# Kernel tuning notes

Hardware: AMD Instinct MI355X
Metric: run time of the kernel (lower is better)

Reference implementation:

```python
import jax, jax.numpy as jnp
import numpy as np

N_LAYERS = 2
NUM_BRANCHES = 3
TOPK_START = 10
TOPK_END = 3


def normalize_adj(adj):
    # symmetric degree normalization: D^-1/2 (A + I) D^-1/2
    n = adj.shape[0]
    a = jnp.clip(adj + jnp.eye(n, dtype=adj.dtype), 1e-8, jnp.inf)
    row_sum = jnp.clip(a.sum(axis=1), 1e-8, jnp.inf)
    d = jnp.clip(row_sum ** -0.5, 0.0, 100.0)
    return d[:, None] * a * d[None, :]


def setup_inputs() -> dict:
    key = jax.random.key(0)
    k1, k2 = jax.random.split(key)
    B, T, N, C = 512, 16, 22, 64
    x = jax.random.normal(k1, (B, T, N, C), dtype=jnp.float32)
    # emulate nn.Parameter init: clamp(adj,0,1)*0.01 + 0.05*I
    raw = jax.random.uniform(k2, (N, N), dtype=jnp.float32)
    adj = jnp.clip(raw, 0.0, 1.0) * 0.01 + 0.05 * jnp.eye(N, dtype=jnp.float32)
    branch_temps = jnp.ones((NUM_BRANCHES,), dtype=jnp.float32)
    fusion_logits = jnp.zeros((N_LAYERS, NUM_BRANCHES), dtype=jnp.float32)
    return {"x": x, "adj": adj, "branch_temps": branch_temps, "fusion_logits": fusion_logits}


def reference(x, adj, branch_temps, fusion_logits):
    B, T, N, C = x.shape
    # [B, T, N, C] -> [B, N, T*C]
    x0 = jnp.transpose(x, (0, 2, 1, 3)).reshape(B, N, T * C)
    A = normalize_adj(jnp.clip(adj, 0.0, 1.0))          # [N, N]
    temps = jnp.clip(branch_temps, 0.1, 10.0)           # [nb]
    eye = jnp.eye(N, dtype=x0.dtype)

    xb = x0
    for layer in range(N_LAYERS):
        K = int(TOPK_START - (TOPK_START - TOPK_END) * (layer / max(1, N_LAYERS - 1)))
        K = min(K, N)
        alpha = jax.nn.softmax(fusion_logits[layer])    # [nb]
        # cosine similarity, masked by normalized adjacency
        xn = xb / (jnp.linalg.norm(xb, axis=-1, keepdims=True) + 1e-6)
        sim = jnp.einsum('bnd,bmd->bnm', xn, xn) * A    # [B, N, N]
        # per-branch temperature + diagonal boost
        att = sim[None] / temps[:, None, None, None] + 0.1 * eye  # [nb, B, N, N]
        # annealed top-k sparsification (zeros still participate in softmax, as in torch)
        _, idx = jax.lax.top_k(att, K)                  # [nb, B, N, K]
        mask = jax.nn.one_hot(idx, N, dtype=att.dtype).sum(axis=-2)  # [nb, B, N, N]
        att = jax.nn.softmax(att * mask, axis=-1)
        y = jnp.einsum('kbnm,bmd->kbnd', att, xb)       # branch aggregation
        xb = jnp.einsum('k,kbnd->bnd', alpha, y)        # fusion
        if layer > 0:
            xb = xb + x0
        if layer < N_LAYERS - 1:
            xb = jax.nn.relu(xb)  # dropout identity in eval mode
    return xb, A
```

## Files before the change

kernel.cpp:

```cpp
#include <hip/hip_runtime.h>
#include <hip/hip_bf16.h>

#define BATCH  512
#define TT     16
#define NN     22
#define CC     64
#define DD     1024
#define NB     3
#define NTHR   512
#define WPAD   40

typedef __bf16 bf16x8 __attribute__((ext_vector_type(8)));
typedef float  f32x4  __attribute__((ext_vector_type(4)));
typedef float  f32x16 __attribute__((ext_vector_type(16)));

__device__ __forceinline__ unsigned bf16rne(float x) {
  unsigned u = __float_as_uint(x);
  u += 0x7fffu + ((u >> 16) & 1u);
  return u >> 16;
}
__device__ __forceinline__ unsigned pack2(float a, float b) {
  return bf16rne(a) | (bf16rne(b) << 16);
}
__device__ __forceinline__ unsigned xoff(unsigned m, unsigned d) {
  return ((d >> 4) * 6u + (m >> 2)) * 64u + (m & 3u) * 16u + (d & 15u);
}

__global__ __launch_bounds__(NTHR) void mbdsca_fused(
    const float* __restrict__ x,
    const float* __restrict__ adj,
    const float* __restrict__ btemps,
    const float* __restrict__ flogits,
    float* __restrict__ out)
{
  __shared__ unsigned short xs[6 * 64 * 64];
  __shared__ float As[NN][NN];
  __shared__ float Gp[4][NN][NN];
  __shared__ float simS[NN][NN];
  __shared__ float attB[NB][NN][NN];
  __shared__ float mxs[NB][NN];
  __shared__ float sinv[NB][NN];
  __shared__ unsigned short Wh[32][WPAD];
  __shared__ unsigned short Wl[32][WPAD];
  __shared__ float deg[NN];
  __shared__ float alphas[2][NB];
  __shared__ float tvals[NB];

  const int tid  = threadIdx.x;
  const int b    = blockIdx.x;
  const int lane = tid & 63;
  const int wv   = tid >> 6;

  if (tid < NN * NN) {
    int n = tid / NN, m = tid - n * NN;
    float v = adj[tid];
    v = fminf(fmaxf(v, 0.0f), 1.0f);
    if (n == m) v += 1.0f;
    As[n][m] = fmaxf(v, 1e-8f);
  }
  if (tid < NB) tvals[tid] = fminf(fmaxf(btemps[tid], 0.1f), 10.0f);
  for (int i = tid; i < 32 * WPAD / 2; i += NTHR) {
    ((unsigned*)Wh)[i] = 0u;
    ((unsigned*)Wl)[i] = 0u;
  }
  __syncthreads();

  if (tid < NN) {
    float s = 0.0f;
    for (int m = 0; m < NN; ++m) s += As[tid][m];
    s = fmaxf(s, 1e-8f);
    deg[tid] = fminf(fmaxf(1.0f / sqrtf(s), 0.0f), 100.0f);
  }
  if (tid == 0) {
    for (int l = 0; l < 2; ++l) {
      float l0 = flogits[l*NB+0], l1 = flogits[l*NB+1], l2 = flogits[l*NB+2];
      float mx = fmaxf(l0, fmaxf(l1, l2));
      float e0 = __expf(l0-mx), e1 = __expf(l1-mx), e2 = __expf(l2-mx);
      float s = e0 + e1 + e2;
      alphas[l][0] = e0/s; alphas[l][1] = e1/s; alphas[l][2] = e2/s;
    }
  }
  __syncthreads();

  if (tid < NN * NN) {
    int n = tid / NN, m = tid - n * NN;
    As[n][m] = deg[n] * As[n][m] * deg[m];
  }
  #pragma unroll
  for (int j = 0; j < 11; ++j) {
    int f4  = tid + j * NTHR;
    int t   = f4 / (NN * (CC/4));
    int rem = f4 - t * (NN * (CC/4));
    int n   = rem >> 4;
    int c4  = rem & 15;
    const float4 v = *(const float4*)(&x[(size_t)b * (TT*NN*CC) + (size_t)f4 * 4]);
    uint2 p; p.x = pack2(v.x, v.y); p.y = pack2(v.z, v.w);
    *(uint2*)(&xs[xoff(n, t * 64 + c4 * 4)]) = p;
  }
  {
    int m  = 22 + (tid >> 8);
    int d0 = (tid & 255) * 4;
    *(uint2*)(&xs[xoff(m, d0)]) = make_uint2(0u, 0u);
  }
  __syncthreads();

  const unsigned xsb = (unsigned)(unsigned long long)(void*)&xs[0];

  for (int layer = 0; layer < 2; ++layer) {
    const int K = (layer == 0) ? 10 : 3;

    if (wv < 4) {
      int row = lane & 31; if (row > NN-1) row = NN-1;
      const int hi = lane >> 5;
      f32x16 acc0 = {}, acc1 = {};
      #pragma unroll
      for (int s = 0; s < 16; ++s) {
        int d0 = (wv * 16 + s) * 16 + hi * 8;
        bf16x8 a = *(const bf16x8*)(&xs[xoff(row, d0)]);
        if (s & 1) acc1 = __builtin_amdgcn_mfma_f32_32x32x16_bf16(a, a, acc1, 0, 0, 0);
        else       acc0 = __builtin_amdgcn_mfma_f32_32x32x16_bf16(a, a, acc0, 0, 0, 0);
      }
      #pragma unroll
      for (int r = 0; r < 16; ++r) {
        float vv = acc0[r] + acc1[r];
        int orow = (r & 3) + 8 * (r >> 2) + 4 * hi;
        int ocol = lane & 31;
        if (orow < NN && ocol < NN) Gp[wv][orow][ocol] = vv;
      }
    }
    __syncthreads();

    if (tid < NN * NN) {
      int n = tid / NN, m = tid - n * NN;
      float g  = Gp[0][n][m] + Gp[1][n][m] + Gp[2][n][m] + Gp[3][n][m];
      float gn = Gp[0][n][n] + Gp[1][n][n] + Gp[2][n][n] + Gp[3][n][n];
      float gm = Gp[0][m][m] + Gp[1][m][m] + Gp[2][m][m] + Gp[3][m][m];
      float rn = 1.0f / (sqrtf(gn) + 1e-6f);
      float rm = 1.0f / (sqrtf(gm) + 1e-6f);
      simS[n][m] = g * rn * rm * As[n][m];
    }
    __syncthreads();

    if (tid < NN * NN) {
      const int n = tid / NN, m = tid - n * NN;
      float simrow[NN];
      float simn = 0.f, simm = 0.f, rmax_ex = -1e30f;
      #pragma unroll
      for (int j = 0; j < NN; ++j) {
        float s = simS[n][j];
        simrow[j] = s;
        simn = (j == n) ? s : simn;
        simm = (j == m) ? s : simm;
        rmax_ex = (j == n) ? rmax_ex : fmaxf(rmax_ex, s);
      }
      #pragma unroll
      for (int k = 0; k < NB; ++k) {
        const float tk  = tvals[k];
        const float rtk = 1.0f / tk;
        const float vn  = simn + 0.1f * tk;
        const float vown = (m == n) ? vn : simm;
        int rank = 0;
        #pragma unroll
        for (int j = 0; j < NN; ++j) {
          float vj = (j == n) ? vn : simrow[j];
          rank += (vj > vown) || (vj == vown && j < m);
        }
        attB[k][n][m] = (rank < K) ? vown * rtk : 0.0f;
        if (m == 0) mxs[k][n] = fmaxf(fmaxf(rmax_ex, vn) * rtk, 0.0f);
      }
    }
    __syncthreads();

    if (tid < NB * NN) {
      int k = tid / NN, n = tid - k * NN;
      float mx = mxs[k][n], s = 0.0f;
      #pragma unroll
      for (int m2 = 0; m2 < NN; ++m2) s += __expf(attB[k][n][m2] - mx);
      sinv[k][n] = alphas[layer][k] / s;
    }
    __syncthreads();

    if (tid < NN * NN) {
      int n = tid / NN, m = tid - n * NN;
      float w = 0.0f;
      #pragma unroll
      for (int k = 0; k < NB; ++k)
        w += __expf(attB[k][n][m] - mxs[k][n]) * sinv[k][n];
      unsigned h = bf16rne(w);
      Wh[n][m] = (unsigned short)h;
      Wl[n][m] = (unsigned short)bf16rne(w - __uint_as_float(h << 16));
    }
    __syncthreads();

    {
      const int n_b = lane & 31;
      const int ko  = (lane >> 5) * 8;
      bf16x8 w0h = *(const bf16x8*)(&Wh[n_b][ko]);
      bf16x8 w0l = *(const bf16x8*)(&Wl[n_b][ko]);
      bf16x8 w1h = *(const bf16x8*)(&Wh[n_b][16 + ko]);
      bf16x8 w1l = *(const bf16x8*)(&Wl[n_b][16 + ko]);
      const int dpr     = lane & 31;
      const int dsub_in = dpr >> 4;
      const int dcol    = dpr & 15;
      const int hi5     = lane >> 5;
      unsigned mqA  = (unsigned)(hi5 * 2);
      unsigned mqB0 = 4 + mqA;  if (mqB0 > 5) mqB0 = 5;
      unsigned mqB1 = 5 + mqA;  if (mqB1 > 5) mqB1 = 5;
      #pragma unroll
      for (int i = 0; i < 4; ++i) {
        const int dtile = wv * 4 + i;
        const unsigned rowb = xsb + (unsigned)(dtile * 2 + dsub_in) * 6u * 128u + (unsigned)dcol * 8u;
        unsigned long long t00, t01, t10, t11;
        asm volatile("ds_read_b64_tr_b16 %0, %1" : "=v"(t00) : "v"(rowb + mqA * 128u));
        asm volatile("ds_read_b64_tr_b16 %0, %1" : "=v"(t01) : "v"(rowb + (mqA + 1u) * 128u));
        asm volatile("ds_read_b64_tr_b16 %0, %1" : "=v"(t10) : "v"(rowb + mqB0 * 128u));
        asm volatile("ds_read_b64_tr_b16 %0, %1" : "=v"(t11) : "v"(rowb + mqB1 * 128u));
        asm volatile("s_waitcnt lgkmcnt(0)" ::: "memory");
        __builtin_amdgcn_sched_barrier(0);
        int4 a0i = make_int4((int)t00, (int)(t00 >> 32), (int)t01, (int)(t01 >> 32));
        int4 a1i = make_int4((int)t10, (int)(t10 >> 32), (int)t11, (int)(t11 >> 32));
        bf16x8 A0 = __builtin_bit_cast(bf16x8, a0i);
        bf16x8 A1 = __builtin_bit_cast(bf16x8, a1i);
        f32x16 acc = {};
        acc = __builtin_amdgcn_mfma_f32_32x32x16_bf16(A0, w0h, acc, 0, 0, 0);
        acc = __builtin_amdgcn_mfma_f32_32x32x16_bf16(A0, w0l, acc, 0, 0, 0);
        acc = __builtin_amdgcn_mfma_f32_32x32x16_bf16(A1, w1h, acc, 0, 0, 0);
        acc = __builtin_amdgcn_mfma_f32_32x32x16_bf16(A1, w1l, acc, 0, 0, 0);
        if (n_b < NN) {
          if (layer == 0) {
            #pragma unroll
            for (int q = 0; q < 4; ++q) {
              int dq = dtile * 32 + 4 * hi5 + 8 * q;
              uint2 p;
              p.x = pack2(fmaxf(acc[4*q+0], 0.f), fmaxf(acc[4*q+1], 0.f));
              p.y = pack2(fmaxf(acc[4*q+2], 0.f), fmaxf(acc[4*q+3], 0.f));
              *(uint2*)(&xs[xoff(n_b, dq)]) = p;
            }
          } else {
            #pragma unroll
            for (int q = 0; q < 4; ++q) {
              int dq = dtile * 32 + 4 * hi5 + 8 * q;
              int t = dq >> 6, c = dq & 63;
              const float4 r = *(const float4*)(&x[(size_t)b * (TT*NN*CC) + (t * NN + n_b) * CC + c]);
              float4 o = make_float4(acc[4*q+0] + r.x, acc[4*q+1] + r.y,
                                     acc[4*q+2] + r.z, acc[4*q+3] + r.w);
              *(float4*)(&out[((size_t)b * NN + n_b) * DD + dq]) = o;
            }
          }
        }
      }
    }
    __syncthreads();
  }

  if (b == 0 && tid < NN * NN) {
    out[(size_t)BATCH * NN * DD + tid] = As[tid / NN][tid - (tid / NN) * NN];
  }
}

extern "C" void kernel_launch(void* const* d_in, const int* in_sizes, int n_in,
                              void* d_out, int out_size, void* d_ws, size_t ws_size,
                              hipStream_t stream) {
  const float* x       = (const float*)d_in[0];
  const float* adj     = (const float*)d_in[1];
  const float* btemps  = (const float*)d_in[2];
  const float* flogits = (const float*)d_in[3];
  float* out = (float*)d_out;
  mbdsca_fused<<<BATCH, NTHR, 0, stream>>>(x, adj, btemps, flogits, out);
}
```

Baseline: 51.66 us.

## Fuse top-k softmax stages into wave-level shuffles and overlap global loads

Replaces the four shared-memory stages (similarity, rank-based top-k, softmax max/sum, weight build) with one stage where each half-wave owns a row and uses shuffles for ranking, max and sum. This drops three block barriers and the simS/attB/mxs/sinv shared buffers. It also issues all global x loads at kernel entry so they overlap the adjacency setup, processes two d-tiles per iteration with interleaved MFMA chains, and raises wave priority around the MFMA blocks. The cost is more shuffle work and register pressure, plus subtle tie-breaking logic in the rank computation.

```diff
diff --git a/kernel.cpp b/kernel.cpp
--- a/kernel.cpp
+++ b/kernel.cpp
@@ -36,10 +36,6 @@
   __shared__ unsigned short xs[6 * 64 * 64];
   __shared__ float As[NN][NN];
   __shared__ float Gp[4][NN][NN];
-  __shared__ float simS[NN][NN];
-  __shared__ float attB[NB][NN][NN];
-  __shared__ float mxs[NB][NN];
-  __shared__ float sinv[NB][NN];
   __shared__ unsigned short Wh[32][WPAD];
   __shared__ unsigned short Wl[32][WPAD];
   __shared__ float deg[NN];
@@ -50,6 +46,12 @@
   const int b    = blockIdx.x;
   const int lane = tid & 63;
   const int wv   = tid >> 6;
+  const float* __restrict__ xb0 = x + (size_t)b * (TT * NN * CC);
+
+  float4 xv[11];
+  #pragma unroll
+  for (int j = 0; j < 11; ++j)
+    xv[j] = *(const float4*)(&xb0[(size_t)(tid + j * NTHR) * 4]);
 
   if (tid < NN * NN) {
     int n = tid / NN, m = tid - n * NN;
@@ -93,8 +95,7 @@
     int rem = f4 - t * (NN * (CC/4));
     int n   = rem >> 4;
     int c4  = rem & 15;
-    const float4 v = *(const float4*)(&x[(size_t)b * (TT*NN*CC) + (size_t)f4 * 4]);
-    uint2 p; p.x = pack2(v.x, v.y); p.y = pack2(v.z, v.w);
+    uint2 p; p.x = pack2(xv[j].x, xv[j].y); p.y = pack2(xv[j].z, xv[j].w);
     *(uint2*)(&xs[xoff(n, t * 64 + c4 * 4)]) = p;
   }
   {
@@ -113,6 +114,7 @@
       int row = lane & 31; if (row > NN-1) row = NN-1;
       const int hi = lane >> 5;
       f32x16 acc0 = {}, acc1 = {};
+      __builtin_amdgcn_s_setprio(1);
       #pragma unroll
       for (int s = 0; s < 16; ++s) {
         int d0 = (wv * 16 + s) * 16 + hi * 8;
@@ -120,6 +122,7 @@
         if (s & 1) acc1 = __builtin_amdgcn_mfma_f32_32x32x16_bf16(a, a, acc1, 0, 0, 0);
         else       acc0 = __builtin_amdgcn_mfma_f32_32x32x16_bf16(a, a, acc0, 0, 0, 0);
       }
+      __builtin_amdgcn_s_setprio(0);
       #pragma unroll
       for (int r = 0; r < 16; ++r) {
         float vv = acc0[r] + acc1[r];
@@ -130,65 +133,74 @@
     }
     __syncthreads();
 
-    if (tid < NN * NN) {
-      int n = tid / NN, m = tid - n * NN;
-      float g  = Gp[0][n][m] + Gp[1][n][m] + Gp[2][n][m] + Gp[3][n][m];
-      float gn = Gp[0][n][n] + Gp[1][n][n] + Gp[2][n][n] + Gp[3][n][n];
-      float gm = Gp[0][m][m] + Gp[1][m][m] + Gp[2][m][m] + Gp[3][m][m];
-      float rn = 1.0f / (sqrtf(gn) + 1e-6f);
-      float rm = 1.0f / (sqrtf(gm) + 1e-6f);
-      simS[n][m] = g * rn * rm * As[n][m];
-    }
-    __syncthreads();
-
-    if (tid < NN * NN) {
-      const int n = tid / NN, m = tid - n * NN;
-      float simrow[NN];
-      float simn = 0.f, simm = 0.f, rmax_ex = -1e30f;
+    {
+      const int j    = lane & 31;
+      const int base = lane & 32;
+      const float t0 = tvals[0], t1 = tvals[1], t2 = tvals[2];
+      const float a0 = alphas[layer][0], a1 = alphas[layer][1], a2 = alphas[layer][2];
       #pragma unroll
-      for (int j = 0; j < NN; ++j) {
-        float s = simS[n][j];
-        simrow[j] = s;
-        simn = (j == n) ? s : simn;
-        simm = (j == m) ? s : simm;
-        rmax_ex = (j == n) ? rmax_ex : fmaxf(rmax_ex, s);
+      for (int pass = 0; pass < 2; ++pass) {
+        const int n = wv * 2 + (lane >> 5) + pass * 16;
+        if (n < NN) {
+          const bool valid = (j < NN);
+          const int  jj    = valid ? j : 0;
+          float g   = Gp[0][n][jj] + Gp[1][n][jj] + Gp[2][n][jj] + Gp[3][n][jj];
+          float gjj = Gp[0][jj][jj] + Gp[1][jj][jj] + Gp[2][jj][jj] + Gp[3][jj][jj];
+          float gnn = Gp[0][n][n]  + Gp[1][n][n]  + Gp[2][n][n]  + Gp[3][n][n];
+          float dj = 1.0f / (sqrtf(gjj) + 1e-6f);
+          float dn = 1.0f / (sqrtf(gnn) + 1e-6f);
+          float v  = g * dn * dj * As[n][jj];
+          if (!valid) v = 0.0f;
+          float vnn = __shfl(v, base + n);
+          float vh0 = vnn + 0.1f * t0;
+          float vh1 = vnn + 0.1f * t1;
+          float vh2 = vnn + 0.1f * t2;
+          int rank = 0, c0 = 0, c1 = 0, c2 = 0;
+          #pragma unroll
+          for (int i = 0; i < NN; ++i) {
+            float vi = __shfl(v, base + i);
+            if (i != n) {
+              rank += ((vi > v)   || (vi == v   && i < j)) ? 1 : 0;
+              c0   += ((vi > vh0) || (vi == vh0 && i < n)) ? 1 : 0;
+              c1   += ((vi > vh1) || (vi == vh1 && i < n)) ? 1 : 0;
+              c2   += ((vi > vh2) || (vi == vh2 && i < n)) ? 1 : 0;
+            }
+          }
+          float w = 0.0f;
+          #pragma unroll
+          for (int k = 0; k < NB; ++k) {
+            const float vh  = (k == 0) ? vh0 : (k == 1) ? vh1 : vh2;
+            const int   cd  = (k == 0) ? c0  : (k == 1) ? c1  : c2;
+            const float tk  = (k == 0) ? t0  : (k == 1) ? t1  : t2;
+            const float ak  = (k == 0) ? a0  : (k == 1) ? a1  : a2;
+            const float rtk = 1.0f / tk;
+            bool dgt = (vh > v) || (vh == v && n < j);
+            int  rk  = (j == n) ? cd : (rank + (dgt ? 1 : 0));
+            bool sel = (rk < K) && valid;
+            float att = sel ? (((j == n) ? vh : v) * rtk) : 0.0f;
+            float mx = att;
+            mx = fmaxf(mx, __shfl_xor(mx, 1));
+            mx = fmaxf(mx, __shfl_xor(mx, 2));
+            mx = fmaxf(mx, __shfl_xor(mx, 4));
+            mx = fmaxf(mx, __shfl_xor(mx, 8));
+            mx = fmaxf(mx, __shfl_xor(mx, 16));
+            mx = fmaxf(mx, 0.0f);
+            float e = valid ? __expf(att - mx) : 0.0f;
+            float s = e;
+            s += __shfl_xor(s, 1);
+            s += __shfl_xor(s, 2);
+            s += __shfl_xor(s, 4);
+            s += __shfl_xor(s, 8);
+            s += __shfl_xor(s, 16);
+            w += e * (ak / s);
+          }
+          if (valid) {
+            unsigned h = bf16rne(w);
+            Wh[n][j] = (unsigned short)h;
+            Wl[n][j] = (unsigned short)bf16rne(w - __uint_as_float(h << 16));
+          }
+        }
       }
-      #pragma unroll
-      for (int k = 0; k < NB; ++k) {
-        const float tk  = tvals[k];
-        const float rtk = 1.0f / tk;
-        const float vn  = simn + 0.1f * tk;
-        const float vown = (m == n) ? vn : simm;
-        int rank = 0;
-        #pragma unroll
-        for (int j = 0; j < NN; ++j) {
-          float vj = (j == n) ? vn : simrow[j];
-          rank += (vj > vown) || (vj == vown && j < m);
-        }
-        attB[k][n][m] = (rank < K) ? vown * rtk : 0.0f;
-        if (m == 0) mxs[k][n] = fmaxf(fmaxf(rmax_ex, vn) * rtk, 0.0f);
-      }
-    }
-    __syncthreads();
-
-    if (tid < NB * NN) {
-      int k = tid / NN, n = tid - k * NN;
-      float mx = mxs[k][n], s = 0.0f;
-      #pragma unroll
-      for (int m2 = 0; m2 < NN; ++m2) s += __expf(attB[k][n][m2] - mx);
-      sinv[k][n] = alphas[layer][k] / s;
-    }
-    __syncthreads();
-
-    if (tid < NN * NN) {
-      int n = tid / NN, m = tid - n * NN;
-      float w = 0.0f;
-      #pragma unroll
-      for (int k = 0; k < NB; ++k)
-        w += __expf(attB[k][n][m] - mxs[k][n]) * sinv[k][n];
-      unsigned h = bf16rne(w);
-      Wh[n][m] = (unsigned short)h;
-      Wl[n][m] = (unsigned short)bf16rne(w - __uint_as_float(h << 16));
     }
     __syncthreads();
 
@@ -207,44 +219,68 @@
       unsigned mqB0 = 4 + mqA;  if (mqB0 > 5) mqB0 = 5;
       unsigned mqB1 = 5 + mqA;  if (mqB1 > 5) mqB1 = 5;
       #pragma unroll
-      for (int i = 0; i < 4; ++i) {
-        const int dtile = wv * 4 + i;
-        const unsigned rowb = xsb + (unsigned)(dtile * 2 + dsub_in) * 6u * 128u + (unsigned)dcol * 8u;
-        unsigned long long t00, t01, t10, t11;
-        asm volatile("ds_read_b64_tr_b16 %0, %1" : "=v"(t00) : "v"(rowb + mqA * 128u));
-        asm volatile("ds_read_b64_tr_b16 %0, %1" : "=v"(t01) : "v"(rowb + (mqA + 1u) * 128u));
-        asm volatile("ds_read_b64_tr_b16 %0, %1" : "=v"(t10) : "v"(rowb + mqB0 * 128u));
-        asm volatile("ds_read_b64_tr_b16 %0, %1" : "=v"(t11) : "v"(rowb + mqB1 * 128u));
+      for (int g = 0; g < 2; ++g) {
+        const int dt0 = wv * 4 + g * 2;
+        const int dt1 = dt0 + 1;
+        const unsigned rb0 = xsb + (unsigned)(dt0 * 2 + dsub_in) * 768u + (unsigned)dcol * 8u;
+        const unsigned rb1 = xsb + (unsigned)(dt1 * 2 + dsub_in) * 768u + (unsigned)dcol * 8u;
+        unsigned long long s00, s01, s02, s03, s10, s11, s12, s13;
+        asm volatile("ds_read_b64_tr_b16 %0, %1" : "=v"(s00) : "v"(rb0 + mqA * 128u));
+        asm volatile("ds_read_b64_tr_b16 %0, %1" : "=v"(s01) : "v"(rb0 + (mqA + 1u) * 128u));
+        asm volatile("ds_read_b64_tr_b16 %0, %1" : "=v"(s02) : "v"(rb0 + mqB0 * 128u));
+        asm volatile("ds_read_b64_tr_b16 %0, %1" : "=v"(s03) : "v"(rb0 + mqB1 * 128u));
+        asm volatile("ds_read_b64_tr_b16 %0, %1" : "=v"(s10) : "v"(rb1 + mqA * 128u));
+        asm volatile("ds_read_b64_tr_b16 %0, %1" : "=v"(s11) : "v"(rb1 + (mqA + 1u) * 128u));
+        asm volatile("ds_read_b64_tr_b16 %0, %1" : "=v"(s12) : "v"(rb1 + mqB0 * 128u));
+        asm volatile("ds_read_b64_tr_b16 %0, %1" : "=v"(s13) : "v"(rb1 + mqB1 * 128u));
         asm volatile("s_waitcnt lgkmcnt(0)" ::: "memory");
         __builtin_amdgcn_sched_barrier(0);
-        int4 a0i = make_int4((int)t00, (int)(t00 >> 32), (int)t01, (int)(t01 >> 32));
-        int4 a1i = make_int4((int)t10, (int)(t10 >> 32), (int)t11, (int)(t11 >> 32));
-        bf16x8 A0 = __builtin_bit_cast(bf16x8, a0i);
-        bf16x8 A1 = __builtin_bit_cast(bf16x8, a1i);
-        f32x16 acc = {};
-        acc = __builtin_amdgcn_mfma_f32_32x32x16_bf16(A0, w0h, acc, 0, 0, 0);
-        acc = __builtin_amdgcn_mfma_f32_32x32x16_bf16(A0, w0l, acc, 0, 0, 0);
-        acc = __builtin_amdgcn_mfma_f32_32x32x16_bf16(A1, w1h, acc, 0, 0, 0);
-        acc = __builtin_amdgcn_mfma_f32_32x32x16_bf16(A1, w1l, acc, 0, 0, 0);
+        int4 a00 = make_int4((int)s00, (int)(s00 >> 32), (int)s01, (int)(s01 >> 32));
+        int4 a01 = make_int4((int)s02, (int)(s02 >> 32), (int)s03, (int)(s03 >> 32));
+        int4 a10 = make_int4((int)s10, (int)(s10 >> 32), (int)s11, (int)(s11 >> 32));
+        int4 a11 = make_int4((int)s12, (int)(s12 >> 32), (int)s13, (int)(s13 >> 32));
+        bf16x8 A00 = __builtin_bit_cast(bf16x8, a00);
+        bf16x8 A01 = __builtin_bit_cast(bf16x8, a01);
+        bf16x8 A10 = __builtin_bit_cast(bf16x8, a10);
+        bf16x8 A11 = __builtin_bit_cast(bf16x8, a11);
+        f32x16 acc0 = {}, acc1 = {};
+        __builtin_amdgcn_s_setprio(1);
+        acc0 = __builtin_amdgcn_mfma_f32_32x32x16_bf16(A00, w0h, acc0, 0, 0, 0);
+        acc1 = __builtin_amdgcn_mfma_f32_32x32x16_bf16(A10, w0h, acc1, 0, 0, 0);
+        acc0 = __builtin_amdgcn_mfma_f32_32x32x16_bf16(A00, w0l, acc0, 0, 0, 0);
+        acc1 = __builtin_amdgcn_mfma_f32_32x32x16_bf16(A10, w0l, acc1, 0, 0, 0);
+        acc0 = __builtin_amdgcn_mfma_f32_32x32x16_bf16(A01, w1h, acc0, 0, 0, 0);
+        acc1 = __builtin_amdgcn_mfma_f32_32x32x16_bf16(A11, w1h, acc1, 0, 0, 0);
+        acc0 = __builtin_amdgcn_mfma_f32_32x32x16_bf16(A01, w1l, acc0, 0, 0, 0);
+        acc1 = __builtin_amdgcn_mfma_f32_32x32x16_bf16(A11, w1l, acc1, 0, 0, 0);
+        __builtin_amdgcn_s_setprio(0);
         if (n_b < NN) {
           if (layer == 0) {
             #pragma unroll
             for (int q = 0; q < 4; ++q) {
-              int dq = dtile * 32 + 4 * hi5 + 8 * q;
-              uint2 p;
-              p.x = pack2(fmaxf(acc[4*q+0], 0.f), fmaxf(acc[4*q+1], 0.f));
-              p.y = pack2(fmaxf(acc[4*q+2], 0.f), fmaxf(acc[4*q+3], 0.f));
-              *(uint2*)(&xs[xoff(n_b, dq)]) = p;
+              int dqa = dt0 * 32 + 4 * hi5 + 8 * q;
+              int dqb = dt1 * 32 + 4 * hi5 + 8 * q;
+              uint2 pa, pb;
+              pa.x = pack2(fmaxf(acc0[4*q+0], 0.f), fmaxf(acc0[4*q+1], 0.f));
+              pa.y = pack2(fmaxf(acc0[4*q+2], 0.f), fmaxf(acc0[4*q+3], 0.f));
+              pb.x = pack2(fmaxf(acc1[4*q+0], 0.f), fmaxf(acc1[4*q+1], 0.f));
+              pb.y = pack2(fmaxf(acc1[4*q+2], 0.f), fmaxf(acc1[4*q+3], 0.f));
+              *(uint2*)(&xs[xoff(n_b, dqa)]) = pa;
+              *(uint2*)(&xs[xoff(n_b, dqb)]) = pb;
             }
           } else {
             #pragma unroll
             for (int q = 0; q < 4; ++q) {
-              int dq = dtile * 32 + 4 * hi5 + 8 * q;
-              int t = dq >> 6, c = dq & 63;
-              const float4 r = *(const float4*)(&x[(size_t)b * (TT*NN*CC) + (t * NN + n_b) * CC + c]);
-              float4 o = make_float4(acc[4*q+0] + r.x, acc[4*q+1] + r.y,
-                                     acc[4*q+2] + r.z, acc[4*q+3] + r.w);
-              *(float4*)(&out[((size_t)b * NN + n_b) * DD + dq]) = o;
+              int dqa = dt0 * 32 + 4 * hi5 + 8 * q;
+              int dqb = dt1 * 32 + 4 * hi5 + 8 * q;
+              const float4 ra = *(const float4*)(&xb0[((dqa >> 6) * NN + n_b) * CC + (dqa & 63)]);
+              const float4 rb = *(const float4*)(&xb0[((dqb >> 6) * NN + n_b) * CC + (dqb & 63)]);
+              *(float4*)(&out[((size_t)b * NN + n_b) * DD + dqa]) =
+                  make_float4(acc0[4*q+0] + ra.x, acc0[4*q+1] + ra.y,
+                              acc0[4*q+2] + ra.z, acc0[4*q+3] + ra.w);
+              *(float4*)(&out[((size_t)b * NN + n_b) * DD + dqb]) =
+                  make_float4(acc1[4*q+0] + rb.x, acc1[4*q+1] + rb.y,
+                              acc1[4*q+2] + rb.z, acc1[4*q+3] + rb.w);
             }
           }
         }
```

New measurement: 63.44 us. 22.8% more time.
